# Optimization experiments

Measured on AMD Instinct MI355X. Metric: run time of the kernel, lower is better.

The kernel has to match this reference:

```python
import jax, jax.numpy as jnp
import numpy as np
from jax import lax

# Static config (matches init_kwargs)
D_MODEL = 1024
EXPAND = 2
D_INNER = D_MODEL * EXPAND          # 2048
HEAD_DIM = 64
N_HEADS = D_INNER // HEAD_DIM       # 32
N_GROUPS = 1
D_STATE = 128
D_CONV = 4
CONV_DIM = D_INNER + 2 * N_GROUPS * D_STATE        # 2304
D_IN_PROJ = 2 * D_INNER + 2 * N_GROUPS * D_STATE + N_HEADS  # 4384
SEQLEN = 8192
LN_EPS = 1e-5


def setup_inputs() -> dict:
    key = jax.random.key(0)
    ks = jax.random.split(key, 6)
    x = jax.random.normal(ks[0], (SEQLEN, D_MODEL), jnp.float32)
    W_in = jax.random.normal(ks[1], (D_IN_PROJ, D_MODEL), jnp.float32) / np.sqrt(D_MODEL)
    W_conv = jax.random.normal(ks[2], (CONV_DIM, 1, D_CONV), jnp.float32) / np.sqrt(D_CONV)
    b_conv = jnp.zeros((CONV_DIM,), jnp.float32)
    # dt_bias init per Mamba2: dt ~ LogUniform(dt_min, dt_max), inverse-softplus
    dt = jnp.exp(jax.random.uniform(ks[3], (N_HEADS,)) * (np.log(0.1) - np.log(0.001)) + np.log(0.001))
    dt = jnp.clip(dt, 1e-4)
    dt_bias = dt + jnp.log(-jnp.expm1(-dt))
    A_log = jnp.log(jax.random.uniform(ks[4], (N_HEADS,), minval=1.0, maxval=16.0))
    D_param = jnp.ones((N_HEADS,), jnp.float32)
    ln_w = jnp.ones((D_INNER,), jnp.float32)
    ln_b = jnp.zeros((D_INNER,), jnp.float32)
    W_out = jax.random.normal(ks[5], (D_MODEL, D_INNER), jnp.float32) / np.sqrt(D_INNER)
    return dict(x=x, W_in=W_in, W_conv=W_conv, b_conv=b_conv, dt_bias=dt_bias,
                A_log=A_log, D_param=D_param, ln_w=ln_w, ln_b=ln_b, W_out=W_out)


def reference(x, W_in, W_conv, b_conv, dt_bias, A_log, D_param, ln_w, ln_b, W_out):
    L = x.shape[0]
    zxbcdt = x @ W_in.T                                   # (L, d_in_proj)
    z = zxbcdt[:, :D_INNER]                               # gate
    xbc = zxbcdt[:, D_INNER:D_INNER + CONV_DIM]           # (L, conv_dim)
    dt = jax.nn.softplus(zxbcdt[:, D_INNER + CONV_DIM:] + dt_bias)  # (L, h)
    # depthwise causal-window conv with SAME padding over the sequence
    lhs = xbc.T[None]                                      # (1, conv_dim, L)
    conv = lax.conv_general_dilated(lhs, W_conv, (1,), 'SAME',
                                    feature_group_count=CONV_DIM,
                                    dimension_numbers=('NCH', 'OIH', 'NCH'))[0]
    xbc = jax.nn.silu((conv + b_conv[:, None]).T)          # (L, conv_dim)
    x_ssm = xbc[:, :D_INNER].reshape(L, N_HEADS, HEAD_DIM)
    B = xbc[:, D_INNER:D_INNER + N_GROUPS * D_STATE].reshape(L, N_GROUPS, D_STATE)
    C = xbc[:, D_INNER + N_GROUPS * D_STATE:].reshape(L, N_GROUPS, D_STATE)
    hpg = N_HEADS // N_GROUPS
    Bh = jnp.repeat(B, hpg, axis=1)                        # (L, h, n)
    Ch = jnp.repeat(C, hpg, axis=1)                        # (L, h, n)
    A = -jnp.exp(A_log)                                    # (h,), negative
    a = jnp.exp(dt * A)                                    # (L, h) per-token decay in (0,1)
    V = x_ssm * dt[..., None]                              # discretized input (L, h, p)
    # non-causal SSD (VSSD): global state H then readout, plus D skip
    H = jnp.einsum('lhn,lh,lhp->hnp', Bh, a, V)            # (h, n, p)
    y = jnp.einsum('lhn,hnp->lhp', Ch, H) + D_param[None, :, None] * x_ssm
    y = y.reshape(L, D_INNER)
    # LayerNorm (eqx default: weight+bias, eps=1e-5), then gate by z
    mu = jnp.mean(y, axis=-1, keepdims=True)
    var = jnp.var(y, axis=-1, keepdims=True)
    y = ((y - mu) / jnp.sqrt(var + LN_EPS)) * ln_w + ln_b
    y = y * z
    return y @ W_out.T                                     # (L, d_model)
```

## Files before the change

### kernel.cpp

```cpp
#include <hip/hip_runtime.h>
#include <hip/hip_bf16.h>
#include <math.h>

#define L_SEQ 8192
#define DM 1024
#define DI 2048
#define NH 32
#define HD 64
#define DS 128
#define CDIM 2304
#define DPROJ 4384
#define NPAD_IN 4480
#define KSPLIT 32
#define OPROWS 2176

typedef short bf16x8 __attribute__((ext_vector_type(8)));
typedef float floatx4 __attribute__((ext_vector_type(4)));
typedef unsigned short u16x4 __attribute__((ext_vector_type(4)));
typedef unsigned short u16x8 __attribute__((ext_vector_type(8)));

#define AS1(p) ((const __attribute__((address_space(1))) void*)(p))
#define AS3(p) ((__attribute__((address_space(3))) void*)(p))

__device__ __forceinline__ float bf2f(unsigned short u) {
  union { unsigned int i; float f; } c; c.i = ((unsigned int)u) << 16; return c.f;
}
__device__ __forceinline__ unsigned short f2bf(float f) {
  return __bfloat16_as_ushort(__float2bfloat16(f));
}

template <int MODE>
__global__ __launch_bounds__(256)
void gemm_bt_mfma(const unsigned short* __restrict__ A, int lda,
                  const unsigned short* __restrict__ B, int ldb,
                  void* __restrict__ Cout, int ldc,
                  int Kfull, int Nstore,
                  const unsigned short* __restrict__ xs,
                  const float* __restrict__ Dvec) {
  __shared__ __align__(16) char smem[17408];
  unsigned short* Asm = (unsigned short*)smem;
  unsigned short* Bsm = Asm + 128 * 32;
  const int t = threadIdx.x;

  int bx = blockIdx.x, by = blockIdx.y;
  if (MODE != 2) {
    int gx = gridDim.x;
    int linear = by * gx + bx;
    int xcd = linear & 7;
    int local = linear >> 3;
    by = xcd * 8 + (local & 7);
    bx = local >> 3;
  }
  const int m0 = by * 128;
  const int n0 = bx * 128;

  int kstart = 0, klen = Kfull;
  if (MODE == 2) { klen = Kfull / KSPLIT; kstart = blockIdx.z * klen; }
  const int wave = t >> 6, lane = t & 63;
  const int wm = (wave & 1) * 64;
  const int wn = (wave >> 1) * 64;
  const int fr = lane & 15;
  const int quad = lane >> 4;

  floatx4 acc[4][4];
#pragma unroll
  for (int i = 0; i < 4; ++i)
#pragma unroll
    for (int j = 0; j < 4; ++j) acc[i][j] = (floatx4){0.f, 0.f, 0.f, 0.f};

  for (int k0 = kstart; k0 < kstart + klen; k0 += 32) {
#pragma unroll
    for (int i = 0; i < 2; ++i) {
      int linear = i * 256 + t;
      int row = linear >> 2;
      int kq = (linear & 3) * 8;
      const unsigned short* ga = A + (size_t)(m0 + row) * lda + (k0 + kq);
      const unsigned short* gb = B + (size_t)(n0 + row) * ldb + (k0 + kq);
      __builtin_amdgcn_global_load_lds(AS1(ga), AS3(&Asm[linear * 8]), 16, 0, 0);
      __builtin_amdgcn_global_load_lds(AS1(gb), AS3(&Bsm[linear * 8]), 16, 0, 0);
    }
    __syncthreads();

    bf16x8 af[4], bfr[4];
#pragma unroll
    for (int i = 0; i < 4; ++i) {
      af[i]  = *(const bf16x8*)&Asm[(wm + i * 16 + fr) * 32 + quad * 8];
      bfr[i] = *(const bf16x8*)&Bsm[(wn + i * 16 + fr) * 32 + quad * 8];
    }
#pragma unroll
    for (int mi = 0; mi < 4; ++mi)
#pragma unroll
      for (int ni = 0; ni < 4; ++ni)
        acc[mi][ni] = __builtin_amdgcn_mfma_f32_16x16x32_bf16(
            af[mi], bfr[ni], acc[mi][ni], 0, 0, 0);
    __syncthreads();
  }

  const int lrbase = (wm ? 16 : 0) + quad * 4;
  if (MODE == 0 || MODE == 1) {
    unsigned short(*rp)[136] = (unsigned short(*)[136])smem;
    unsigned short* C = (unsigned short*)Cout;
#pragma unroll
    for (int mi = 0; mi < 4; ++mi) {
      __syncthreads();
#pragma unroll
      for (int ni = 0; ni < 4; ++ni)
#pragma unroll
        for (int r = 0; r < 4; ++r)
          rp[lrbase + r][wn + ni * 16 + fr] = f2bf(acc[mi][ni][r]);
      __syncthreads();
#pragma unroll
      for (int j = 0; j < 2; ++j) {
        int off = j * 2048 + t * 8;
        int lr = off >> 7, c = off & 127;
        int grow = m0 + (lr >> 4) * 64 + mi * 16 + (lr & 15);
        int gcol = n0 + c;
        u16x8 v = *(const u16x8*)&rp[lr][c];
        if (MODE == 1) {
          u16x8 xv = *(const u16x8*)&xs[(size_t)grow * ldc + gcol];
          float Dh = Dvec[gcol >> 6];
          u16x8 o;
#pragma unroll
          for (int e = 0; e < 8; ++e) o[e] = f2bf(bf2f(v[e]) + Dh * bf2f(xv[e]));
          *(u16x8*)&C[(size_t)grow * ldc + gcol] = o;
        } else {
          if (gcol < Nstore) *(u16x8*)&C[(size_t)grow * ldc + gcol] = v;
        }
      }
    }
  } else {
    float(*rpf)[136] = (float(*)[136])smem;
    float* C = (float*)Cout;
    if (MODE == 2) C += (size_t)blockIdx.z * DS * DI;
#pragma unroll
    for (int mi = 0; mi < 4; ++mi) {
      __syncthreads();
#pragma unroll
      for (int ni = 0; ni < 4; ++ni)
#pragma unroll
        for (int r = 0; r < 4; ++r)
          rpf[lrbase + r][wn + ni * 16 + fr] = acc[mi][ni][r];
      __syncthreads();
#pragma unroll
      for (int j = 0; j < 4; ++j) {
        int off = j * 1024 + t * 4;
        int lr = off >> 7, c = off & 127;
        int grow = m0 + (lr >> 4) * 64 + mi * 16 + (lr & 15);
        int gcol = n0 + c;
        float4 v = *(const float4*)&rpf[lr][c];
        *(float4*)&C[(size_t)grow * ldc + gcol] = v;
      }
    }
  }
}

__global__ __launch_bounds__(256)
void cast_all_kernel(const float* __restrict__ x, const float* __restrict__ W_in,
                     const float* __restrict__ W_out,
                     unsigned short* __restrict__ x_bf16,
                     unsigned short* __restrict__ win_bf16,
                     unsigned short* __restrict__ wout_bf16) {
  int b = blockIdx.x;
  int t = threadIdx.x;
  u16x4 o = (u16x4){0, 0, 0, 0};
  if (b < 8192) {
    size_t i4 = ((size_t)b * 256 + t) * 4;
    float4 v = *(const float4*)(x + i4);
    o.x = f2bf(v.x); o.y = f2bf(v.y); o.z = f2bf(v.z); o.w = f2bf(v.w);
    *(u16x4*)(x_bf16 + i4) = o;
  } else if (b < 12672) {
    size_t i4 = ((size_t)(b - 8192) * 256 + t) * 4;
    int row = (int)(i4 >> 10);
    if (row < DPROJ) {
      float4 v = *(const float4*)(W_in + i4);
      o.x = f2bf(v.x); o.y = f2bf(v.y); o.z = f2bf(v.z); o.w = f2bf(v.w);
    }
    *(u16x4*)(win_bf16 + i4) = o;
  } else {
    size_t i4 = ((size_t)(b - 12672) * 256 + t) * 4;
    float4 v = *(const float4*)(W_out + i4);
    o.x = f2bf(v.x); o.y = f2bf(v.y); o.z = f2bf(v.z); o.w = f2bf(v.w);
    *(u16x4*)(wout_bf16 + i4) = o;
  }
}

__global__ __launch_bounds__(256)
void dt_kernel(const unsigned short* __restrict__ zxb, const float* __restrict__ dt_bias,
               const float* __restrict__ A_log, float* __restrict__ s_out) {
  int idx = blockIdx.x * 256 + threadIdx.x;
  int l = idx >> 5, h = idx & 31;
  float v = bf2f(zxb[(size_t)l * DPROJ + (DI + CDIM) + h]) + dt_bias[h];
  float d = (v > 20.f) ? v : log1pf(expf(v));
  s_out[idx] = d * expf(-d * expf(A_log[h]));
}

__global__ __launch_bounds__(256)
void conv_fused_kernel(const unsigned short* __restrict__ zxb,
                       const float* __restrict__ Wc,
                       const float* __restrict__ bc,
                       const float* __restrict__ svec,
                       unsigned short* __restrict__ xs,
                       unsigned short* __restrict__ cb,
                       unsigned short* __restrict__ OpT) {
  __shared__ unsigned short zt[67][66];
  __shared__ unsigned short ot[64][66];
  __shared__ float sl[64];
  const int c0 = blockIdx.x * 64;
  const int l0 = blockIdx.y * 64;
  const int t = threadIdx.x;
  for (int idx = t; idx < 67 * 16; idx += 256) {
    int row = idx >> 4;
    int colq = (idx & 15) * 4;
    int gl = l0 - 1 + row;
    u16x4 v = (u16x4){0, 0, 0, 0};
    if (gl >= 0 && gl < L_SEQ)
      v = *(const u16x4*)&zxb[(size_t)gl * DPROJ + DI + c0 + colq];
    *(u16x4*)&zt[row][colq] = v;
  }
  const bool isX = (c0 < DI);
  const bool isC = (c0 >= DI + DS);
  if (isX && t < 64) sl[t] = svec[(size_t)(l0 + t) * NH + (c0 >> 6)];
  const int c = t & 63;
  const int gc = c0 + c;
  const float4 wv = *(const float4*)&Wc[gc * 4];
  const float bias = bc[gc];
  const int lq = (t >> 6) * 16;
  __syncthreads();
#pragma unroll
  for (int i = 0; i < 16; ++i) {
    int ll = lq + i;
    float sacc = bias + bf2f(zt[ll][c]) * wv.x + bf2f(zt[ll + 1][c]) * wv.y +
                 bf2f(zt[ll + 2][c]) * wv.z + bf2f(zt[ll + 3][c]) * wv.w;
    float v = sacc / (1.f + expf(-sacc));
    int gl = l0 + ll;
    if (isC) {
      cb[(size_t)gl * DS + (gc - (DI + DS))] = f2bf(v);
    } else if (isX) {
      xs[(size_t)gl * DI + gc] = f2bf(v);
      ot[c][ll] = f2bf(v * sl[ll]);
    } else {
      ot[c][ll] = f2bf(v);
    }
  }
  if (!isC) {
    __syncthreads();
#pragma unroll
    for (int j = 0; j < 4; ++j) {
      int linear = j * 1024 + t * 4;
      int rr = linear >> 6;
      int lc = linear & 63;
      *(u16x4*)&OpT[(size_t)(c0 + rr) * L_SEQ + l0 + lc] = *(const u16x4*)&ot[rr][lc];
    }
  }
}

__global__ __launch_bounds__(256)
void h_reduce_t_kernel(const float* __restrict__ P, unsigned short* __restrict__ Ht) {
  __shared__ float tile[32][65];
  const int bid = blockIdx.x;
  const int pt = bid & 31, ng = bid >> 5;
  const int t = threadIdx.x;
#pragma unroll
  for (int i = 0; i < 8; ++i) {
    int nl = i * 4 + (t >> 6);
    int n = ng * 32 + nl;
    int p = pt * 64 + (t & 63);
    float acc = 0.f;
#pragma unroll
    for (int z = 0; z < KSPLIT; ++z)
      acc += P[(size_t)z * (DS * DI) + (size_t)n * DI + p];
    tile[nl][t & 63] = acc;
  }
  __syncthreads();
#pragma unroll
  for (int j = 0; j < 8; ++j) {
    int linear = j * 256 + t;
    int pl = linear >> 5, nl = linear & 31;
    Ht[(size_t)(pt * 64 + pl) * DS + ng * 32 + nl] = f2bf(tile[nl][pl]);
  }
}

__global__ __launch_bounds__(256)
void ln_mul_kernel(const unsigned short* __restrict__ ybuf, unsigned short* __restrict__ zxb,
                   const float* __restrict__ ln_w, const float* __restrict__ ln_b) {
  int l = blockIdx.x;
  int t = threadIdx.x;
  int c0 = t * 8;
  u16x8 yv = *(const u16x8*)&ybuf[(size_t)l * DI + c0];
  float vals[8];
  float s = 0.f, sq = 0.f;
#pragma unroll
  for (int i = 0; i < 8; ++i) {
    float v = bf2f(yv[i]);
    vals[i] = v;
    s += v;
    sq += v * v;
  }
#pragma unroll
  for (int off = 32; off > 0; off >>= 1) {
    s += __shfl_down(s, off, 64);
    sq += __shfl_down(sq, off, 64);
  }
  __shared__ float red[10];
  int wave = t >> 6, lane = t & 63;
  if (lane == 0) { red[wave] = s; red[4 + wave] = sq; }
  __syncthreads();
  if (t == 0) {
    float S = red[0] + red[1] + red[2] + red[3];
    float SQ = red[4] + red[5] + red[6] + red[7];
    float mu = S / (float)DI;
    red[8] = mu;
    red[9] = rsqrtf(SQ / (float)DI - mu * mu + 1e-5f);
  }
  __syncthreads();
  float mu = red[8], rstd = red[9];
  unsigned short* zrow = zxb + (size_t)l * DPROJ;
  u16x8 zv = *(const u16x8*)&zrow[c0];
  float4 w0 = *(const float4*)&ln_w[c0], w1 = *(const float4*)&ln_w[c0 + 4];
  float4 b0 = *(const float4*)&ln_b[c0], b1 = *(const float4*)&ln_b[c0 + 4];
  float w[8] = {w0.x, w0.y, w0.z, w0.w, w1.x, w1.y, w1.z, w1.w};
  float b[8] = {b0.x, b0.y, b0.z, b0.w, b1.x, b1.y, b1.z, b1.w};
  u16x8 o;
#pragma unroll
  for (int i = 0; i < 8; ++i) {
    float v = (vals[i] - mu) * rstd * w[i] + b[i];
    o[i] = f2bf(v * bf2f(zv[i]));
  }
  *(u16x8*)&zrow[DI + c0] = o;
}

extern "C" void kernel_launch(void* const* d_in, const int* in_sizes, int n_in,
                              void* d_out, int out_size, void* d_ws, size_t ws_size,
                              hipStream_t stream) {
  const float* x       = (const float*)d_in[0];
  const float* W_in    = (const float*)d_in[1];
  const float* W_conv  = (const float*)d_in[2];
  const float* b_conv  = (const float*)d_in[3];
  const float* dt_bias = (const float*)d_in[4];
  const float* A_log   = (const float*)d_in[5];
  const float* D_param = (const float*)d_in[6];
  const float* ln_w    = (const float*)d_in[7];
  const float* ln_b    = (const float*)d_in[8];
  const float* W_out   = (const float*)d_in[9];
  float* out = (float*)d_out;

  unsigned short* zxb = (unsigned short*)d_ws;
  unsigned short* xs   = zxb + (size_t)L_SEQ * DPROJ;
  unsigned short* cb   = xs + (size_t)L_SEQ * DI;
  float* svec = (float*)(cb + (size_t)L_SEQ * DS);
  unsigned short* OpT = (unsigned short*)(svec + (size_t)L_SEQ * NH);
  float* Ppart = (float*)(OpT + (size_t)OPROWS * L_SEQ);
  unsigned short* Ht = (unsigned short*)(Ppart + (size_t)KSPLIT * DS * DI);
  unsigned short* wout_bf16 = Ht + (size_t)DI * DS;
  unsigned short* x_bf16   = OpT;
  unsigned short* win_bf16 = OpT + (size_t)L_SEQ * DM;
  unsigned short* ybuf     = OpT;

  cast_all_kernel<<<14720, 256, 0, stream>>>(x, W_in, W_out, x_bf16, win_bf16,
                                             wout_bf16);

  gemm_bt_mfma<0><<<dim3(NPAD_IN / 128, L_SEQ / 128), 256, 0, stream>>>(
      x_bf16, DM, win_bf16, DM, zxb, DPROJ, DM, DPROJ, nullptr, nullptr);

  dt_kernel<<<(L_SEQ * NH) / 256, 256, 0, stream>>>(zxb, dt_bias, A_log, svec);

  conv_fused_kernel<<<dim3(CDIM / 64, L_SEQ / 64), 256, 0, stream>>>(
      zxb, W_conv, b_conv, svec, xs, cb, OpT);

  gemm_bt_mfma<2><<<dim3(DI / 128, 1, KSPLIT), 256, 0, stream>>>(
      OpT + (size_t)DI * L_SEQ, L_SEQ, OpT, L_SEQ, Ppart, DI, L_SEQ, DI,
      nullptr, nullptr);

  h_reduce_t_kernel<<<128, 256, 0, stream>>>(Ppart, Ht);

  gemm_bt_mfma<1><<<dim3(DI / 128, L_SEQ / 128), 256, 0, stream>>>(
      cb, DS, Ht, DS, ybuf, DI, DS, DI, xs, D_param);

  ln_mul_kernel<<<L_SEQ, 256, 0, stream>>>(ybuf, zxb, ln_w, ln_b);

  gemm_bt_mfma<3><<<dim3(DM / 128, L_SEQ / 128), 256, 0, stream>>>(
      zxb + DI, DPROJ, wout_bf16, DI, out, DM, DI, DM, nullptr, nullptr);
}
```

Before: 370.5 us.

## Replace input projection GEMM with 256x256 tiled 8-phase pipelined MFMA kernel

```diff
diff --git a/kernel.cpp b/kernel.cpp
--- a/kernel.cpp
+++ b/kernel.cpp
@@ -10,7 +10,7 @@
 #define DS 128
 #define CDIM 2304
 #define DPROJ 4384
-#define NPAD_IN 4480
+#define NPAD_IN 4608
 #define KSPLIT 32
 #define OPROWS 2176
 
@@ -27,6 +27,176 @@
 }
 __device__ __forceinline__ unsigned short f2bf(float f) {
   return __bfloat16_as_ushort(__float2bfloat16(f));
+}
+
+__global__ __launch_bounds__(512, 2)
+void gemm256_8ph(const unsigned short* __restrict__ A, int lda,
+                 const unsigned short* __restrict__ B, int ldb,
+                 unsigned short* __restrict__ C, int ldc,
+                 int K, int Nstore) {
+  __shared__ __align__(16) char lds[131072];
+  const int t = threadIdx.x;
+  const int lane = t & 63;
+  const int w = t >> 6;
+  const int wm = w & 1, wn = w >> 1;
+  const int fr = lane & 15, quad = lane >> 4;
+
+  int gx = gridDim.x, gy = gridDim.y;
+  int linear = blockIdx.y * gx + blockIdx.x;
+  int xcd = linear & 7, loc = linear >> 3;
+  int mper = gy >> 3;
+  int mt = xcd * mper + loc % mper;
+  int nt = loc / mper;
+  const int m0 = mt << 8, n0 = nt << 8;
+  const int NT = K >> 6;
+
+  floatx4 acc[8][4];
+#pragma unroll
+  for (int i = 0; i < 8; ++i)
+#pragma unroll
+    for (int j = 0; j < 4; ++j) acc[i][j] = (floatx4){0.f, 0.f, 0.f, 0.f};
+  bf16x8 af[4][2], b0[2][2], b1[2][2];
+
+  auto stA = [&](int buf, int kt, int g) {
+#pragma unroll
+    for (int i = 0; i < 2; ++i) {
+      int o = (i * 512 + t) * 16;
+      int os = o ^ (((o >> 7) & 7) << 4);
+      int rloc = os >> 7, kb = os & 127;
+      int R = ((rloc >> 6) << 7) | (g << 6) | (rloc & 63);
+      const unsigned short* src = A + (size_t)(m0 + R) * lda + (kt << 6) + (kb >> 1);
+      __builtin_amdgcn_global_load_lds(AS1(src),
+          AS3(lds + buf * 32768 + g * 16384 + o), 16, 0, 0);
+    }
+  };
+  auto stB = [&](int buf, int kt, int g) {
+#pragma unroll
+    for (int i = 0; i < 2; ++i) {
+      int o = (i * 512 + t) * 16;
+      int os = o ^ (((o >> 7) & 7) << 4);
+      int rloc = os >> 7, kb = os & 127;
+      int R = ((rloc >> 5) << 6) | (g << 5) | (rloc & 31);
+      const unsigned short* src = B + (size_t)(n0 + R) * ldb + (kt << 6) + (kb >> 1);
+      __builtin_amdgcn_global_load_lds(AS1(src),
+          AS3(lds + 65536 + buf * 32768 + g * 16384 + o), 16, 0, 0);
+    }
+  };
+  auto rdA = [&](int buf, int mi, int ks) -> bf16x8 {
+    int rloc = (wm << 6) | ((mi & 3) << 4) | fr;
+    return *(const bf16x8*)(lds + buf * 32768 + (mi >> 2) * 16384 + rloc * 128 +
+                            (((ks << 6) | (quad << 4)) ^ ((fr & 7) << 4)));
+  };
+  auto rdB = [&](int buf, int ni, int ks) -> bf16x8 {
+    int rloc = (wn << 5) | ((ni & 1) << 4) | fr;
+    return *(const bf16x8*)(lds + 65536 + buf * 32768 + (ni >> 1) * 16384 + rloc * 128 +
+                            (((ks << 6) | (quad << 4)) ^ ((fr & 7) << 4)));
+  };
+
+  stA(0, 0, 0); stB(0, 0, 0); stB(0, 0, 1); stA(0, 0, 1);
+  if (NT > 1) { stA(1, 1, 0); stB(1, 1, 0); stB(1, 1, 1); }
+  if (NT > 1) asm volatile("s_waitcnt vmcnt(6)" ::: "memory");
+  else        asm volatile("s_waitcnt vmcnt(0)" ::: "memory");
+  __builtin_amdgcn_sched_barrier(0);
+  __builtin_amdgcn_s_barrier();
+
+  for (int kt = 0; kt < NT; ++kt) {
+    const int buf = kt & 1;
+    const bool pf1 = (kt + 1 < NT);
+    const bool pf2 = (kt + 2 < NT);
+#pragma unroll
+    for (int mi = 0; mi < 4; ++mi) { af[mi][0] = rdA(buf, mi, 0); af[mi][1] = rdA(buf, mi, 1); }
+#pragma unroll
+    for (int ni = 0; ni < 2; ++ni) { b0[ni][0] = rdB(buf, ni, 0); b0[ni][1] = rdB(buf, ni, 1); }
+    if (pf1) stA(buf ^ 1, kt + 1, 1);
+    __builtin_amdgcn_sched_barrier(0);
+    __builtin_amdgcn_s_barrier();
+    asm volatile("s_waitcnt lgkmcnt(0)" ::: "memory");
+    __builtin_amdgcn_sched_barrier(0);
+    __builtin_amdgcn_s_setprio(1);
+#pragma unroll
+    for (int mi = 0; mi < 4; ++mi)
+#pragma unroll
+      for (int ni = 0; ni < 2; ++ni)
+#pragma unroll
+        for (int ks = 0; ks < 2; ++ks)
+          acc[mi][ni] = __builtin_amdgcn_mfma_f32_16x16x32_bf16(af[mi][ks], b0[ni][ks], acc[mi][ni], 0, 0, 0);
+    __builtin_amdgcn_s_setprio(0);
+    __builtin_amdgcn_sched_barrier(0);
+    __builtin_amdgcn_s_barrier();
+#pragma unroll
+    for (int ni = 0; ni < 2; ++ni) { b1[ni][0] = rdB(buf, ni + 2, 0); b1[ni][1] = rdB(buf, ni + 2, 1); }
+    if (pf2) stA(buf, kt + 2, 0);
+    __builtin_amdgcn_sched_barrier(0);
+    __builtin_amdgcn_s_barrier();
+    asm volatile("s_waitcnt lgkmcnt(0)" ::: "memory");
+    __builtin_amdgcn_sched_barrier(0);
+    __builtin_amdgcn_s_setprio(1);
+#pragma unroll
+    for (int mi = 0; mi < 4; ++mi)
+#pragma unroll
+      for (int ni = 0; ni < 2; ++ni)
+#pragma unroll
+        for (int ks = 0; ks < 2; ++ks)
+          acc[mi][ni + 2] = __builtin_amdgcn_mfma_f32_16x16x32_bf16(af[mi][ks], b1[ni][ks], acc[mi][ni + 2], 0, 0, 0);
+    __builtin_amdgcn_s_setprio(0);
+    __builtin_amdgcn_sched_barrier(0);
+    __builtin_amdgcn_s_barrier();
+#pragma unroll
+    for (int mi = 0; mi < 4; ++mi) { af[mi][0] = rdA(buf, mi + 4, 0); af[mi][1] = rdA(buf, mi + 4, 1); }
+    if (pf2) stB(buf, kt + 2, 0);
+    __builtin_amdgcn_sched_barrier(0);
+    __builtin_amdgcn_s_barrier();
+    asm volatile("s_waitcnt lgkmcnt(0)" ::: "memory");
+    __builtin_amdgcn_sched_barrier(0);
+    __builtin_amdgcn_s_setprio(1);
+#pragma unroll
+    for (int mi = 0; mi < 4; ++mi)
+#pragma unroll
+      for (int ni = 0; ni < 2; ++ni)
+#pragma unroll
+        for (int ks = 0; ks < 2; ++ks)
+          acc[mi + 4][ni + 2] = __builtin_amdgcn_mfma_f32_16x16x32_bf16(af[mi][ks], b1[ni][ks], acc[mi + 4][ni + 2], 0, 0, 0);
+    __builtin_amdgcn_s_setprio(0);
+    __builtin_amdgcn_sched_barrier(0);
+    __builtin_amdgcn_s_barrier();
+    if (pf2) stB(buf, kt + 2, 1);
+    __builtin_amdgcn_sched_barrier(0);
+    __builtin_amdgcn_s_barrier();
+    __builtin_amdgcn_s_setprio(1);
+#pragma unroll
+    for (int mi = 0; mi < 4; ++mi)
+#pragma unroll
+      for (int ni = 0; ni < 2; ++ni)
+#pragma unroll
+        for (int ks = 0; ks < 2; ++ks)
+          acc[mi + 4][ni] = __builtin_amdgcn_mfma_f32_16x16x32_bf16(af[mi][ks], b0[ni][ks], acc[mi + 4][ni], 0, 0, 0);
+    __builtin_amdgcn_s_setprio(0);
+    __builtin_amdgcn_sched_barrier(0);
+    if (kt < NT - 1) {
+      if (pf2) asm volatile("s_waitcnt vmcnt(6)" ::: "memory");
+      else     asm volatile("s_waitcnt vmcnt(0)" ::: "memory");
+      __builtin_amdgcn_s_barrier();
+    }
+  }
+
+  unsigned short* rp = (unsigned short*)lds;
+  const int mb = wm * 128, nb = wn * 64;
+#pragma unroll
+  for (int mi = 0; mi < 8; ++mi)
+#pragma unroll
+    for (int ni = 0; ni < 4; ++ni)
+#pragma unroll
+      for (int r = 0; r < 4; ++r)
+        rp[(mb + mi * 16 + quad * 4 + r) * 256 + nb + ni * 16 + fr] = f2bf(acc[mi][ni][r]);
+  __syncthreads();
+#pragma unroll
+  for (int j = 0; j < 16; ++j) {
+    int lin = j * 4096 + t * 8;
+    int row = lin >> 8, col = lin & 255;
+    int gcol = n0 + col;
+    if (gcol < Nstore)
+      *(u16x8*)&C[(size_t)(m0 + row) * ldc + gcol] = *(const u16x8*)&rp[lin];
+  }
 }
 
 template <int MODE>
@@ -168,7 +338,7 @@
     float4 v = *(const float4*)(x + i4);
     o.x = f2bf(v.x); o.y = f2bf(v.y); o.z = f2bf(v.z); o.w = f2bf(v.w);
     *(u16x4*)(x_bf16 + i4) = o;
-  } else if (b < 12672) {
+  } else if (b < 12800) {
     size_t i4 = ((size_t)(b - 8192) * 256 + t) * 4;
     int row = (int)(i4 >> 10);
     if (row < DPROJ) {
@@ -177,7 +347,7 @@
     }
     *(u16x4*)(win_bf16 + i4) = o;
   } else {
-    size_t i4 = ((size_t)(b - 12672) * 256 + t) * 4;
+    size_t i4 = ((size_t)(b - 12800) * 256 + t) * 4;
     float4 v = *(const float4*)(W_out + i4);
     o.x = f2bf(v.x); o.y = f2bf(v.y); o.z = f2bf(v.z); o.w = f2bf(v.w);
     *(u16x4*)(wout_bf16 + i4) = o;
@@ -356,11 +526,11 @@
   unsigned short* win_bf16 = OpT + (size_t)L_SEQ * DM;
   unsigned short* ybuf     = OpT;
 
-  cast_all_kernel<<<14720, 256, 0, stream>>>(x, W_in, W_out, x_bf16, win_bf16,
+  cast_all_kernel<<<14848, 256, 0, stream>>>(x, W_in, W_out, x_bf16, win_bf16,
                                              wout_bf16);
 
-  gemm_bt_mfma<0><<<dim3(NPAD_IN / 128, L_SEQ / 128), 256, 0, stream>>>(
-      x_bf16, DM, win_bf16, DM, zxb, DPROJ, DM, DPROJ, nullptr, nullptr);
+  gemm256_8ph<<<dim3(NPAD_IN / 256, L_SEQ / 256), 512, 0, stream>>>(
+      x_bf16, DM, win_bf16, DM, zxb, DPROJ, DM, DPROJ);
 
   dt_kernel<<<(L_SEQ * NH) / 256, 256, 0, stream>>>(zxb, dt_bias, A_log, svec);
 
```

Measured after the change: 362.8 us. 1.02x faster.
